# Kernel optimization log

Hardware: AMD Instinct MI355X
Metric: run time of the kernel (lower is better)

## Reference

```python
import jax, jax.numpy as jnp
import numpy as np

K = 8  # search_range in sample_wise_recolor
BIG = 1e30


def setup_inputs() -> dict:
    key = jax.random.key(0)
    ks = jax.random.split(key, 6)
    L, N = 16384, 10000  # L: upsampled candidate voxels (multiple of 8), N: target points
    pred_F = jax.random.normal(ks[0], (L,), jnp.float32)
    cand_xyz = jax.random.normal(ks[1], (L, 3), jnp.float32) * 50.0
    cand_rgb = jax.random.uniform(ks[2], (L, 3), jnp.float32)
    tgt_xyz = jax.random.normal(ks[3], (N, 3), jnp.float32) * 50.0
    tgt_rgb = jax.random.uniform(ks[4], (N, 3), jnp.float32)
    keep_target = jax.random.randint(ks[5], (L,), 0, 2, jnp.int32)
    return {"pred_F": pred_F, "cand_xyz": cand_xyz, "cand_rgb": cand_rgb,
            "tgt_xyz": tgt_xyz, "tgt_rgb": tgt_rgb, "keep_target": keep_target,
            "points_num": 8192}


def _get_keep(pred, points_num):
    # local-max mask over groups of 8 children (scatter of per-row argmax)
    L = pred.shape[0]
    p8 = pred.reshape(-1, 8)
    rows = jnp.arange(p8.shape[0])
    is_local_max = jnp.zeros(p8.shape, dtype=bool).at[rows, jnp.argmax(p8, axis=1)].set(True).reshape(-1)
    # kthvalue over the non-local-max subset: local-max entries pushed to +inf so the
    # k-th smallest of the full sorted array equals the k-th smallest of the subset.
    k = L - points_num  # static python int
    vals = jnp.where(is_local_max, jnp.inf, pred)
    threshold = jnp.sort(vals)[k - 1]
    return (pred > threshold) | is_local_max


def _pairwise_sqdist(a, b):
    # a: [P,3], b: [Q,3] -> [P,Q] squared distances
    a2 = jnp.sum(a * a, axis=1)
    b2 = jnp.sum(b * b, axis=1)
    d2 = a2[:, None] + b2[None, :] - 2.0 * (a @ b.T)
    return jnp.maximum(d2, 0.0)


def _recolor_loss(cand_xyz, rgb, keep, tgt_xyz, tgt_rgb):
    L = cand_xyz.shape[0]
    N = tgt_xyz.shape[0]
    d2 = _pairwise_sqdist(tgt_xyz, cand_xyz)  # [N, L]

    # ---- recolor_backward: KNN from each target point into kept candidates ----
    d_masked = jnp.where(keep[None, :], d2, BIG)
    neg_d, idx = jax.lax.top_k(-d_masked, K)  # [N, K]
    d = -neg_d
    zero_mask = d == 0.0
    min_mask = (d == jnp.min(d, axis=1, keepdims=True)) & ~jnp.any(zero_mask, axis=1)[:, None]
    w = jnp.where(min_mask, 1.0 / jnp.sqrt(jnp.maximum(d, 1e-30)), 0.0)  # [N, K]

    flat_idx = idx.reshape(-1)
    num = jnp.zeros((L, 3), rgb.dtype).at[flat_idx].add((tgt_rgb[:, None, :] * w[:, :, None]).reshape(-1, 3))
    den = jnp.zeros((L,), rgb.dtype).at[flat_idx].add(w.reshape(-1))
    has_den = den != 0.0
    recolored = jnp.where(has_den[:, None], num / jnp.where(has_den, den, 1.0)[:, None], 0.0)

    # exact-match (zero-distance) targets overwrite; scatter with safe out-of-range dummy row
    safe_idx = jnp.where(zero_mask, idx, L).reshape(-1)
    tgt_exp = jnp.broadcast_to(tgt_rgb[:, None, :], (N, K, 3)).reshape(-1, 3)
    recolored = jnp.concatenate([recolored, jnp.zeros((1, 3), rgb.dtype)], 0).at[safe_idx].set(tgt_exp)[:L]
    empty = jnp.concatenate([~has_den, jnp.zeros((1,), bool)], 0).at[safe_idx].set(False)[:L]
    empty = empty & keep  # only kept candidates matter

    # ---- recolor_forward: kept candidates with no color yet pull from nearest targets ----
    neg_df, idxf = jax.lax.top_k(-d2.T, K)  # [L, K]
    df = -neg_df
    mf = df == jnp.min(df, axis=1, keepdims=True)
    rec_fwd = jnp.sum(tgt_rgb[idxf] * mf[:, :, None], axis=1) / jnp.sum(mf, axis=1, keepdims=True).astype(rgb.dtype)
    recolored = jnp.where(empty[:, None], rec_fwd, recolored)

    # L1 loss over kept candidates only; recolor target is no-grad in the original
    recolored = jax.lax.stop_gradient(recolored)
    return jnp.sum(jnp.where(keep[:, None], jnp.abs(rgb - recolored), 0.0))


def reference(pred_F, cand_xyz, cand_rgb, tgt_xyz, tgt_rgb, keep_target, points_num):
    keep = _get_keep(jax.lax.stop_gradient(pred_F), points_num)  # @torch.no_grad
    # coord recon loss: BCE-with-logits, reduction='sum'
    t = keep_target.astype(pred_F.dtype)
    coord_loss = jnp.sum(jnp.maximum(pred_F, 0.0) - pred_F * t + jnp.log1p(jnp.exp(-jnp.abs(pred_F))))
    # inverse_transform_for_color in training mode: x * 255
    rgb = cand_rgb * 255.0
    rgb_loss = _recolor_loss(cand_xyz, rgb, keep, tgt_xyz, tgt_rgb)
    return jnp.stack([coord_loss, rgb_loss])
```

## Files before the change

kernel.cpp:

```cpp
#include <hip/hip_runtime.h>
#include <hip/hip_bf16.h>


#define SCAN_T 256
#define CHUNK  128
typedef unsigned long long ull;

__global__ __launch_bounds__(256) void k_prep(
    const float* __restrict__ pred, const float* __restrict__ txyz,
    float4* __restrict__ ttile, float4* __restrict__ numden,
    int* __restrict__ zerohit, ull* __restrict__ tmin, ull* __restrict__ fmin,
    unsigned int* __restrict__ key, unsigned char* __restrict__ islm,
    int* __restrict__ counters, float* __restrict__ out, int L, int N) {
  int gidx = blockIdx.x * 256 + threadIdx.x;
  int gsz = (int)gridDim.x * 256;
  for (int i = gidx; i < N; i += gsz) {
    float x = txyz[3*i], y = txyz[3*i+1], z = txyz[3*i+2];
    ttile[i] = make_float4(x, y, z, fmaf(x, x, fmaf(y, y, z * z)));
    tmin[i] = ~0ull;
  }
  for (int i = gidx; i < L; i += gsz) {
    numden[i] = make_float4(0.f, 0.f, 0.f, 0.f);
    zerohit[i] = 0;
    fmin[i] = ~0ull;
  }
  if (gidx < 8) counters[gidx] = 0;
  if (gidx < 2) out[gidx] = 0.f;
  int ngroups = L >> 3;
  for (int g = gidx; g < ngroups; g += gsz) {
    const float4* pv = (const float4*)pred + (size_t)g * 2;
    float4 a = pv[0], b = pv[1];
    float v[8] = {a.x, a.y, a.z, a.w, b.x, b.y, b.z, b.w};
    int bi = 0; float bv = v[0];
    #pragma unroll
    for (int j = 1; j < 8; ++j) if (v[j] > bv) { bv = v[j]; bi = j; }
    unsigned int kk[8];
    ull lmpack = 0ull;
    #pragma unroll
    for (int j = 0; j < 8; ++j) {
      unsigned int fb = __float_as_uint(v[j]);
      unsigned int mk = (fb & 0x80000000u) ? ~fb : (fb | 0x80000000u);
      if (j == bi) { mk = 0xFF800000u; lmpack |= 1ull << (8 * j); }
      kk[j] = mk;
    }
    ((uint4*)key)[g*2]   = make_uint4(kk[0], kk[1], kk[2], kk[3]);
    ((uint4*)key)[g*2+1] = make_uint4(kk[4], kk[5], kk[6], kk[7]);
    *(ull*)(islm + (size_t)g * 8) = lmpack;
  }
}

__device__ __forceinline__ void select_bin(
    unsigned int* hist, int nb, unsigned int rank,
    unsigned int* sB, unsigned int* sR, int tid) {
  if (tid < 64) {
    int g = nb >> 6;
    unsigned int sum = 0;
    for (int j = 0; j < g; ++j) sum += hist[tid * g + j];
    unsigned int incl = sum;
    for (int o = 1; o < 64; o <<= 1) {
      unsigned int v = __shfl_up(incl, o);
      if (tid >= o) incl += v;
    }
    unsigned int excl = incl - sum;
    bool cond = (rank >= excl) && (rank < incl);
    unsigned long long bal = __ballot(cond);
    int first = __ffsll((long long)bal) - 1;
    if (tid == first) {
      unsigned int r = rank - excl, cum = 0;
      for (int j = 0; j < g; ++j) {
        unsigned int c = hist[tid * g + j];
        if (r < cum + c) { *sB = (unsigned int)(tid * g + j); *sR = r - cum; break; }
        cum += c;
      }
    }
  }
}

__global__ __launch_bounds__(256) void k_sel(
    const unsigned int* __restrict__ key, const int* __restrict__ pnum_p,
    float* __restrict__ thr_out, int L) {
  __shared__ unsigned int hist[2048];
  __shared__ unsigned int sB, sR;
  int tid = threadIdx.x;
  unsigned int rank = (unsigned int)(L - pnum_p[0] - 1);
  const uint4* k4 = (const uint4*)key;
  int n4 = L >> 2;
  for (int b = tid; b < 2048; b += 256) hist[b] = 0u;
  __syncthreads();
  for (int i = tid; i < n4; i += 256) {
    uint4 v = k4[i];
    atomicAdd(&hist[v.x >> 21], 1u); atomicAdd(&hist[v.y >> 21], 1u);
    atomicAdd(&hist[v.z >> 21], 1u); atomicAdd(&hist[v.w >> 21], 1u);
  }
  __syncthreads();
  select_bin(hist, 2048, rank, &sB, &sR, tid);
  __syncthreads();
  unsigned int B1 = sB, R1 = sR;
  for (int b = tid; b < 2048; b += 256) hist[b] = 0u;
  __syncthreads();
  for (int i = tid; i < n4; i += 256) {
    uint4 v = k4[i];
    if ((v.x >> 21) == B1) atomicAdd(&hist[(v.x >> 10) & 2047u], 1u);
    if ((v.y >> 21) == B1) atomicAdd(&hist[(v.y >> 10) & 2047u], 1u);
    if ((v.z >> 21) == B1) atomicAdd(&hist[(v.z >> 10) & 2047u], 1u);
    if ((v.w >> 21) == B1) atomicAdd(&hist[(v.w >> 10) & 2047u], 1u);
  }
  __syncthreads();
  select_bin(hist, 2048, R1, &sB, &sR, tid);
  __syncthreads();
  unsigned int B2 = sB, R2 = sR;
  for (int b = tid; b < 1024; b += 256) hist[b] = 0u;
  __syncthreads();
  unsigned int top22 = (B1 << 11) | B2;
  for (int i = tid; i < n4; i += 256) {
    uint4 v = k4[i];
    if ((v.x >> 10) == top22) atomicAdd(&hist[v.x & 1023u], 1u);
    if ((v.y >> 10) == top22) atomicAdd(&hist[v.y & 1023u], 1u);
    if ((v.z >> 10) == top22) atomicAdd(&hist[v.z & 1023u], 1u);
    if ((v.w >> 10) == top22) atomicAdd(&hist[v.w & 1023u], 1u);
  }
  __syncthreads();
  select_bin(hist, 1024, R2, &sB, &sR, tid);
  __syncthreads();
  if (tid == 0) {
    unsigned int fkey = (B1 << 21) | (B2 << 10) | sB;
    unsigned int fb = (fkey & 0x80000000u) ? (fkey & 0x7FFFFFFFu) : ~fkey;
    thr_out[0] = __uint_as_float(fb);
  }
}

__global__ __launch_bounds__(256) void k_keepc(
    const float* __restrict__ pred, const unsigned char* __restrict__ islm,
    const float* __restrict__ thr_p, const float* __restrict__ cxyz,
    const int* __restrict__ ktgt, int* __restrict__ keep,
    float4* __restrict__ klist, int* __restrict__ kidx,
    int* __restrict__ counters, float* __restrict__ out, int L) {
  int i = blockIdx.x * 256 + threadIdx.x;
  float thr = thr_p[0];
  float term = 0.f;
  if (i < L) {
    float p = pred[i];
    bool kp = (p > thr) || islm[i];
    keep[i] = kp ? 1 : 0;
    if (kp) {
      int pos = atomicAdd(&counters[0], 1);
      float x = cxyz[3*i], y = cxyz[3*i+1], z = cxyz[3*i+2];
      klist[pos] = make_float4(x, y, z, fmaf(x, x, fmaf(y, y, z * z)));
      kidx[pos] = i;
    }
    float t = (float)ktgt[i];
    term = fmaxf(p, 0.f) - p * t + log1pf(expf(-fabsf(p)));
  }
  for (int o = 32; o > 0; o >>= 1) term += __shfl_down(term, o);
  if ((threadIdx.x & 63) == 0) atomicAdd(&out[0], term);
}

__global__ __launch_bounds__(SCAN_T) void k_scan2(
    const float* __restrict__ txyz, const float4* __restrict__ klist,
    const int* __restrict__ kidx, const float4* __restrict__ ttile,
    const int* __restrict__ counters, ull* __restrict__ tmin,
    ull* __restrict__ fmin, int L, int N, int YB) {
  __shared__ float4 tile[CHUNK];
  int tid = threadIdx.x, x = blockIdx.x, y = blockIdx.y;
  int kc = counters[0];

  if (y < YB) {
    int c0 = y * CHUNK;
    if (x * 1024 >= N || c0 >= kc) return;
    int cnt = min(CHUNK, kc - c0);
    if (tid < cnt) tile[tid] = klist[c0 + tid];
    __syncthreads();
    int tb = x * 1024 + tid;
    float ntx[4], nty[4], ntz[4], best[4];
    int bpos[4];
    bool act[4];
    #pragma unroll
    for (int j = 0; j < 4; ++j) {
      int t = tb + 256 * j;
      act[j] = t < N;
      float tx = 0.f, ty = 0.f, tz = 0.f;
      if (act[j]) { tx = txyz[3*t]; ty = txyz[3*t+1]; tz = txyz[3*t+2]; }
      ntx[j] = -2.f * tx; nty[j] = -2.f * ty; ntz[j] = -2.f * tz;
      best[j] = 3e38f; bpos[j] = 0;
    }
    #pragma unroll 4
    for (int c = 0; c < cnt; ++c) {
      float4 cd = tile[c];
      #pragma unroll
      for (int j = 0; j < 4; ++j) {
        float d = fmaf(ntx[j], cd.x, cd.w);
        d = fmaf(nty[j], cd.y, d);
        d = fmaf(ntz[j], cd.z, d);
        if (d < best[j]) { best[j] = d; bpos[j] = c; }
      }
    }
    #pragma unroll
    for (int j = 0; j < 4; ++j) {
      if (act[j]) {
        int p = c0 + bpos[j];
        float4 cd = klist[p];
        float tx = -0.5f * ntx[j], ty = -0.5f * nty[j], tz = -0.5f * ntz[j];
        float dx = tx - cd.x, dy = ty - cd.y, dz = tz - cd.z;
        float dtrue = fmaf(dx, dx, fmaf(dy, dy, dz * dz));
        ull pack = ((ull)__float_as_uint(dtrue) << 32) | (unsigned int)kidx[p];
        atomicMin(&tmin[tb + 256 * j], pack);
      }
    }
  } else {
    int t0 = (y - YB) * CHUNK;
    if (x * 1024 >= kc || t0 >= N) return;
    int tcnt = min(CHUNK, N - t0);
    if (tid < tcnt) tile[tid] = ttile[t0 + tid];
    __syncthreads();
    int eb = x * 1024 + tid;
    float ncx[4], ncy[4], ncz[4], c2[4], best[4];
    int bpos[4], li[4];
    bool act[4];
    #pragma unroll
    for (int j = 0; j < 4; ++j) {
      int e = eb + 256 * j;
      act[j] = e < kc;
      float cx = 0.f, cy = 0.f, cz = 0.f;
      c2[j] = 0.f; li[j] = 0;
      if (act[j]) {
        float4 cd = klist[e];
        cx = cd.x; cy = cd.y; cz = cd.z; c2[j] = cd.w;
        li[j] = kidx[e];
      }
      ncx[j] = -2.f * cx; ncy[j] = -2.f * cy; ncz[j] = -2.f * cz;
      best[j] = 3e38f; bpos[j] = 0;
    }
    #pragma unroll 4
    for (int c = 0; c < tcnt; ++c) {
      float4 td = tile[c];
      #pragma unroll
      for (int j = 0; j < 4; ++j) {
        float d = fmaf(ncx[j], td.x, td.w);
        d = fmaf(ncy[j], td.y, d);
        d = fmaf(ncz[j], td.z, d);
        if (d < best[j]) { best[j] = d; bpos[j] = c; }
      }
    }
    #pragma unroll
    for (int j = 0; j < 4; ++j) {
      if (act[j]) {
        float dkey = fmaxf(best[j] + c2[j], 0.f);
        ull pack = ((ull)__float_as_uint(dkey) << 32) |
                   (unsigned int)(t0 + bpos[j]);
        atomicMin(&fmin[li[j]], pack);
      }
    }
  }
}

__global__ __launch_bounds__(256) void k_scatter(
    const float* __restrict__ trgb, const ull* __restrict__ tmin,
    float4* __restrict__ numden, int* __restrict__ zerohit,
    float4* __restrict__ zcolor, int N) {
  int t = blockIdx.x * 256 + threadIdx.x;
  if (t >= N) return;
  ull pack = tmin[t];
  float d = __uint_as_float((unsigned int)(pack >> 32));
  int idx = (int)(pack & 0xFFFFFFFFull);
  float r = trgb[3*t], g = trgb[3*t+1], b = trgb[3*t+2];
  if (d == 0.0f) {
    zerohit[idx] = 1;
    zcolor[idx] = make_float4(r, g, b, 0.f);
  } else {
    float w = 1.0f / sqrtf(fmaxf(d, 1e-30f));
    atomicAdd(&numden[idx].x, r * w);
    atomicAdd(&numden[idx].y, g * w);
    atomicAdd(&numden[idx].z, b * w);
    atomicAdd(&numden[idx].w, w);
  }
}

__global__ __launch_bounds__(256) void k_loss(
    const float* __restrict__ crgb, const float* __restrict__ trgb,
    const int* __restrict__ keep, const float4* __restrict__ numden,
    const int* __restrict__ zerohit, const float4* __restrict__ zcolor,
    const ull* __restrict__ fmin, float* __restrict__ out, int L) {
  int l = blockIdx.x * 256 + threadIdx.x;
  float loss = 0.f;
  if (l < L && keep[l]) {
    float rr, rg, rb;
    if (zerohit[l]) {
      float4 z = zcolor[l]; rr = z.x; rg = z.y; rb = z.z;
    } else {
      float4 nd = numden[l];
      if (nd.w != 0.f) { rr = nd.x / nd.w; rg = nd.y / nd.w; rb = nd.z / nd.w; }
      else {
        int ti = (int)(fmin[l] & 0xFFFFFFFFull);
        rr = trgb[3*ti]; rg = trgb[3*ti+1]; rb = trgb[3*ti+2];
      }
    }
    float sr = crgb[3*l]*255.f, sg = crgb[3*l+1]*255.f, sb = crgb[3*l+2]*255.f;
    loss = fabsf(sr - rr) + fabsf(sg - rg) + fabsf(sb - rb);
  }
  for (int o = 32; o > 0; o >>= 1) loss += __shfl_down(loss, o);
  if ((threadIdx.x & 63) == 0) atomicAdd(&out[1], loss);
}

extern "C" void kernel_launch(void* const* d_in, const int* in_sizes, int n_in,
                              void* d_out, int out_size, void* d_ws, size_t ws_size,
                              hipStream_t stream) {
  const float* pred = (const float*)d_in[0];
  const float* cxyz = (const float*)d_in[1];
  const float* crgb = (const float*)d_in[2];
  const float* txyz = (const float*)d_in[3];
  const float* trgb = (const float*)d_in[4];
  const int*   ktgt = (const int*)d_in[5];
  const int*   pnum = (const int*)d_in[6];
  int L = in_sizes[0];
  int N = in_sizes[3] / 3;

  char* ws = (char*)d_ws;
  size_t off = 0;
  float4* klist  = (float4*)(ws + off);   off += (size_t)L * 16;
  float4* ttile  = (float4*)(ws + off);   off += (size_t)((N + 3) & ~3) * 16;
  float4* numden = (float4*)(ws + off);   off += (size_t)L * 16;
  float4* zcolor = (float4*)(ws + off);   off += (size_t)L * 16;
  unsigned int* key = (unsigned int*)(ws + off); off += (size_t)L * 4;
  ull* tmin      = (ull*)(ws + off);      off += (size_t)((N + 1) & ~1) * 8;
  ull* fmin      = (ull*)(ws + off);      off += (size_t)L * 8;
  int* keep      = (int*)(ws + off);      off += (size_t)L * 4;
  int* kidx      = (int*)(ws + off);      off += (size_t)L * 4;
  int* zerohit   = (int*)(ws + off);      off += (size_t)L * 4;
  float* thr_slot = (float*)(ws + off);   off += 16;
  int* counters  = (int*)(ws + off);      off += 256;
  unsigned char* islm = (unsigned char*)(ws + off); off += ((size_t)L + 15) & ~15ull;
  float* out = (float*)d_out;

  int nbL = (L + 255) / 256;
  int nbN = (N + 255) / 256;
  int mx = max(L, N);

  k_prep<<<(mx + 255) / 256, 256, 0, stream>>>(
      pred, txyz, ttile, numden, zerohit, tmin, fmin, key, islm, counters, out, L, N);

  k_sel<<<1, 256, 0, stream>>>(key, pnum, thr_slot, L);

  k_keepc<<<nbL, 256, 0, stream>>>(
      pred, islm, thr_slot, cxyz, ktgt, keep, klist, kidx, counters, out, L);

  int gx = (mx + 1023) / 1024;
  int YB = (L + CHUNK - 1) / CHUNK;
  int YF = (N + CHUNK - 1) / CHUNK;
  dim3 gs(gx, YB + YF);
  k_scan2<<<gs, SCAN_T, 0, stream>>>(
      txyz, klist, kidx, ttile, counters, tmin, fmin, L, N, YB);

  k_scatter<<<nbN, 256, 0, stream>>>(trgb, tmin, numden, zerohit, zcolor, N);

  k_loss<<<nbL, 256, 0, stream>>>(
      crgb, trgb, keep, numden, zerohit, zcolor, fmin, out, L);
}
```

Baseline: 140.5 us.

## Fuse init and threshold selection into one kernel with LDS-resident keys

Merges the prep kernel and the single-block radix-select kernel into one launch. Most blocks do the buffer initialisation, while one extra 512-thread block computes the local-max keys directly into 64 KB of shared memory and runs the three histogram passes from LDS instead of re-reading global memory. This removes one kernel launch and the global key round-trip. In exchange, every block now reserves the large shared array even though only one uses it, and the selection still runs serially on a single block. The code also hard-codes L at most 16384 for the shared key array.

```diff
diff --git a/kernel.cpp b/kernel.cpp
--- a/kernel.cpp
+++ b/kernel.cpp
@@ -5,49 +5,6 @@
 #define SCAN_T 256
 #define CHUNK  128
 typedef unsigned long long ull;
-
-__global__ __launch_bounds__(256) void k_prep(
-    const float* __restrict__ pred, const float* __restrict__ txyz,
-    float4* __restrict__ ttile, float4* __restrict__ numden,
-    int* __restrict__ zerohit, ull* __restrict__ tmin, ull* __restrict__ fmin,
-    unsigned int* __restrict__ key, unsigned char* __restrict__ islm,
-    int* __restrict__ counters, float* __restrict__ out, int L, int N) {
-  int gidx = blockIdx.x * 256 + threadIdx.x;
-  int gsz = (int)gridDim.x * 256;
-  for (int i = gidx; i < N; i += gsz) {
-    float x = txyz[3*i], y = txyz[3*i+1], z = txyz[3*i+2];
-    ttile[i] = make_float4(x, y, z, fmaf(x, x, fmaf(y, y, z * z)));
-    tmin[i] = ~0ull;
-  }
-  for (int i = gidx; i < L; i += gsz) {
-    numden[i] = make_float4(0.f, 0.f, 0.f, 0.f);
-    zerohit[i] = 0;
-    fmin[i] = ~0ull;
-  }
-  if (gidx < 8) counters[gidx] = 0;
-  if (gidx < 2) out[gidx] = 0.f;
-  int ngroups = L >> 3;
-  for (int g = gidx; g < ngroups; g += gsz) {
-    const float4* pv = (const float4*)pred + (size_t)g * 2;
-    float4 a = pv[0], b = pv[1];
-    float v[8] = {a.x, a.y, a.z, a.w, b.x, b.y, b.z, b.w};
-    int bi = 0; float bv = v[0];
-    #pragma unroll
-    for (int j = 1; j < 8; ++j) if (v[j] > bv) { bv = v[j]; bi = j; }
-    unsigned int kk[8];
-    ull lmpack = 0ull;
-    #pragma unroll
-    for (int j = 0; j < 8; ++j) {
-      unsigned int fb = __float_as_uint(v[j]);
-      unsigned int mk = (fb & 0x80000000u) ? ~fb : (fb | 0x80000000u);
-      if (j == bi) { mk = 0xFF800000u; lmpack |= 1ull << (8 * j); }
-      kk[j] = mk;
-    }
-    ((uint4*)key)[g*2]   = make_uint4(kk[0], kk[1], kk[2], kk[3]);
-    ((uint4*)key)[g*2+1] = make_uint4(kk[4], kk[5], kk[6], kk[7]);
-    *(ull*)(islm + (size_t)g * 8) = lmpack;
-  }
-}
 
 __device__ __forceinline__ void select_bin(
     unsigned int* hist, int nb, unsigned int rank,
@@ -76,19 +33,64 @@
   }
 }
 
-__global__ __launch_bounds__(256) void k_sel(
-    const unsigned int* __restrict__ key, const int* __restrict__ pnum_p,
-    float* __restrict__ thr_out, int L) {
+__global__ __launch_bounds__(512) void k_init_sel(
+    const float* __restrict__ pred, const float* __restrict__ txyz,
+    const int* __restrict__ pnum_p,
+    float4* __restrict__ ttile, float4* __restrict__ numden,
+    int* __restrict__ zerohit, ull* __restrict__ tmin, ull* __restrict__ fmin,
+    unsigned char* __restrict__ islm, int* __restrict__ counters,
+    float* __restrict__ out, float* __restrict__ thr_out,
+    int L, int N, int IB) {
+  __shared__ unsigned int skey[16384];
   __shared__ unsigned int hist[2048];
   __shared__ unsigned int sB, sR;
   int tid = threadIdx.x;
+
+  if ((int)blockIdx.x < IB) {
+    int gidx = blockIdx.x * 512 + tid;
+    int gsz = IB * 512;
+    for (int i = gidx; i < N; i += gsz) {
+      float x = txyz[3*i], y = txyz[3*i+1], z = txyz[3*i+2];
+      ttile[i] = make_float4(x, y, z, fmaf(x, x, fmaf(y, y, z * z)));
+      tmin[i] = ~0ull;
+    }
+    for (int i = gidx; i < L; i += gsz) {
+      numden[i] = make_float4(0.f, 0.f, 0.f, 0.f);
+      zerohit[i] = 0;
+      fmin[i] = ~0ull;
+    }
+    if (gidx < 8) counters[gidx] = 0;
+    if (gidx < 2) out[gidx] = 0.f;
+    return;
+  }
+
+  int ngroups = L >> 3;
+  for (int g = tid; g < ngroups; g += 512) {
+    const float4* pv = (const float4*)pred + (size_t)g * 2;
+    float4 a = pv[0], b = pv[1];
+    float v[8] = {a.x, a.y, a.z, a.w, b.x, b.y, b.z, b.w};
+    int bi = 0; float bv = v[0];
+    #pragma unroll
+    for (int j = 1; j < 8; ++j) if (v[j] > bv) { bv = v[j]; bi = j; }
+    ull lmpack = 0ull;
+    #pragma unroll
+    for (int j = 0; j < 8; ++j) {
+      unsigned int fb = __float_as_uint(v[j]);
+      unsigned int mk = (fb & 0x80000000u) ? ~fb : (fb | 0x80000000u);
+      if (j == bi) { mk = 0xFF800000u; lmpack |= 1ull << (8 * j); }
+      skey[g * 8 + j] = mk;
+    }
+    *(ull*)(islm + (size_t)g * 8) = lmpack;
+  }
+  __syncthreads();
+
   unsigned int rank = (unsigned int)(L - pnum_p[0] - 1);
-  const uint4* k4 = (const uint4*)key;
+  const uint4* s4 = (const uint4*)skey;
   int n4 = L >> 2;
-  for (int b = tid; b < 2048; b += 256) hist[b] = 0u;
-  __syncthreads();
-  for (int i = tid; i < n4; i += 256) {
-    uint4 v = k4[i];
+  for (int b = tid; b < 2048; b += 512) hist[b] = 0u;
+  __syncthreads();
+  for (int i = tid; i < n4; i += 512) {
+    uint4 v = s4[i];
     atomicAdd(&hist[v.x >> 21], 1u); atomicAdd(&hist[v.y >> 21], 1u);
     atomicAdd(&hist[v.z >> 21], 1u); atomicAdd(&hist[v.w >> 21], 1u);
   }
@@ -96,10 +98,10 @@
   select_bin(hist, 2048, rank, &sB, &sR, tid);
   __syncthreads();
   unsigned int B1 = sB, R1 = sR;
-  for (int b = tid; b < 2048; b += 256) hist[b] = 0u;
-  __syncthreads();
-  for (int i = tid; i < n4; i += 256) {
-    uint4 v = k4[i];
+  for (int b = tid; b < 2048; b += 512) hist[b] = 0u;
+  __syncthreads();
+  for (int i = tid; i < n4; i += 512) {
+    uint4 v = s4[i];
     if ((v.x >> 21) == B1) atomicAdd(&hist[(v.x >> 10) & 2047u], 1u);
     if ((v.y >> 21) == B1) atomicAdd(&hist[(v.y >> 10) & 2047u], 1u);
     if ((v.z >> 21) == B1) atomicAdd(&hist[(v.z >> 10) & 2047u], 1u);
@@ -109,11 +111,11 @@
   select_bin(hist, 2048, R1, &sB, &sR, tid);
   __syncthreads();
   unsigned int B2 = sB, R2 = sR;
-  for (int b = tid; b < 1024; b += 256) hist[b] = 0u;
+  for (int b = tid; b < 1024; b += 512) hist[b] = 0u;
   __syncthreads();
   unsigned int top22 = (B1 << 11) | B2;
-  for (int i = tid; i < n4; i += 256) {
-    uint4 v = k4[i];
+  for (int i = tid; i < n4; i += 512) {
+    uint4 v = s4[i];
     if ((v.x >> 10) == top22) atomicAdd(&hist[v.x & 1023u], 1u);
     if ((v.y >> 10) == top22) atomicAdd(&hist[v.y & 1023u], 1u);
     if ((v.z >> 10) == top22) atomicAdd(&hist[v.z & 1023u], 1u);
@@ -320,7 +322,6 @@
   float4* ttile  = (float4*)(ws + off);   off += (size_t)((N + 3) & ~3) * 16;
   float4* numden = (float4*)(ws + off);   off += (size_t)L * 16;
   float4* zcolor = (float4*)(ws + off);   off += (size_t)L * 16;
-  unsigned int* key = (unsigned int*)(ws + off); off += (size_t)L * 4;
   ull* tmin      = (ull*)(ws + off);      off += (size_t)((N + 1) & ~1) * 8;
   ull* fmin      = (ull*)(ws + off);      off += (size_t)L * 8;
   int* keep      = (int*)(ws + off);      off += (size_t)L * 4;
@@ -335,10 +336,10 @@
   int nbN = (N + 255) / 256;
   int mx = max(L, N);
 
-  k_prep<<<(mx + 255) / 256, 256, 0, stream>>>(
-      pred, txyz, ttile, numden, zerohit, tmin, fmin, key, islm, counters, out, L, N);
-
-  k_sel<<<1, 256, 0, stream>>>(key, pnum, thr_slot, L);
+  int IB = (mx + 511) / 512;
+  k_init_sel<<<IB + 1, 512, 0, stream>>>(
+      pred, txyz, pnum, ttile, numden, zerohit, tmin, fmin, islm, counters,
+      out, thr_slot, L, N, IB);
 
   k_keepc<<<nbL, 256, 0, stream>>>(
       pred, islm, thr_slot, cxyz, ktgt, keep, klist, kidx, counters, out, L);
```

New measurement: 132.4 us. 1.06x faster.
